# Performance work log

Hardware: AMD Instinct MI355X
Metric: run time of the kernel (lower is better)

Reference implementation:

```python
import jax, jax.numpy as jnp
import numpy as np
import math

N_HEADS = 4
GELU = lambda x: jax.nn.gelu(x, approximate=False)  # torch nn.GELU default = exact erf

def _ln(x, s, b):
    m = jnp.mean(x, axis=-1, keepdims=True)
    v = jnp.mean((x - m) ** 2, axis=-1, keepdims=True)
    return (x - m) * jax.lax.rsqrt(v + 1e-5) * s + b

def _fwd(materials, in_seq, proj_vars, param_vars, enc_w1, enc_b1, enc_w2, enc_b2, sos,
         tl_wq, tl_wk, tl_wv, tl_bq, tl_bk, tl_bv, tl_wo, tl_bo,
         tl_ln1s, tl_ln1b, tl_ln2s, tl_ln2b, tl_fw1, tl_fb1, tl_fw2, tl_fb2,
         pw1, pb1, pw2, pb2, pw3, pb3, pw4, pb4, pw5, pb5,
         ipw1, ipb1, ipw2, ipb2, hw1, hb1, hw2, hb2, hw3, hb3):
    B = in_seq.shape[0]
    # encoder input MLP: [B,S,1] -> [B,S,D]
    x = GELU(in_seq @ enc_w1 + enc_b1) @ enc_w2 + enc_b2
    x = jnp.concatenate([jnp.broadcast_to(sos, (B, 1, sos.shape[-1])), x], axis=1)
    S1, D = x.shape[1], x.shape[2]
    dh = D // N_HEADS
    # sinusoidal positional encoding
    pos = jnp.arange(S1, dtype=jnp.float32)[:, None]
    div = jnp.exp(jnp.arange(0, D, 2, dtype=jnp.float32) * (-math.log(10000.0) / D))
    ang = pos * div
    pe = jnp.stack([jnp.sin(ang), jnp.cos(ang)], axis=-1).reshape(S1, D)
    x = x + pe
    scale = 1.0 / math.sqrt(dh)
    # post-LN TransformerEncoder layers (torch default norm_first=False), eval mode (no dropout)
    for l in range(tl_wq.shape[0]):
        q = (x @ tl_wq[l] + tl_bq[l]).reshape(B, S1, N_HEADS, dh).transpose(0, 2, 1, 3)
        k = (x @ tl_wk[l] + tl_bk[l]).reshape(B, S1, N_HEADS, dh).transpose(0, 2, 1, 3)
        v = (x @ tl_wv[l] + tl_bv[l]).reshape(B, S1, N_HEADS, dh).transpose(0, 2, 1, 3)
        att = jax.nn.softmax(jnp.einsum('bhqd,bhkd->bhqk', q, k) * scale, axis=-1)
        o = jnp.einsum('bhqk,bhkd->bhqd', att, v).transpose(0, 2, 1, 3).reshape(B, S1, D)
        x = _ln(x + o @ tl_wo[l] + tl_bo[l], tl_ln1s[l], tl_ln1b[l])
        f = GELU(x @ tl_fw1[l] + tl_fb1[l]) @ tl_fw2[l] + tl_fb2[l]
        x = _ln(x + f, tl_ln2s[l], tl_ln2b[l])
    sos_out = x[:, 0]
    h = jnp.concatenate([proj_vars, sos_out], axis=1)
    for w, b in ((pw1, pb1), (pw2, pb2), (pw3, pb3), (pw4, pb4)):
        h = GELU(h @ w + b)
    proj_out = h @ pw5 + pb5
    pp = GELU(param_vars @ ipw1 + ipb1) @ ipw2 + ipb2
    mi = jnp.concatenate([pp, proj_out], axis=1)  # [B, output_features+param_vars]
    # MaterialHead mask-gather-MLP-scatter == run every tiny head densely, pick by material id
    h1 = GELU(jnp.einsum('bi,mio->mbo', mi, hw1) + hb1[:, None, :])
    h2 = GELU(jnp.einsum('mbi,mio->mbo', h1, hw2) + hb2[:, None, :])
    h3 = jnp.einsum('mbi,mio->mbo', h2, hw3) + hb3[:, None, :]  # [M,B,1]
    return h3[materials, jnp.arange(B)]  # [B,1]

def setup_inputs() -> dict:
    key = jax.random.key(0)
    ks = iter(jax.random.split(key, 64))
    def rn(shape, scale=0.05):
        return jax.random.normal(next(ks), shape, dtype=jnp.float32) * scale
    B, S, IN, EL, D, L, DFF = 64, 1024, 1, 48, 64, 3, 256
    PV, PP, OF, M = 3, 3, 24, 3
    IF = OF + PP
    return dict(
        in_seq=rn((B, S, IN), 1.0),
        proj_vars=rn((B, PV), 1.0),
        param_vars=rn((B, PP), 1.0),
        materials=jax.random.randint(next(ks), (B,), 0, M),
        enc_w1=rn((IN, EL)), enc_b1=rn((EL,)), enc_w2=rn((EL, D)), enc_b2=rn((D,)),
        sos=rn((1, 1, D)),
        tl_wq=rn((L, D, D)), tl_wk=rn((L, D, D)), tl_wv=rn((L, D, D)),
        tl_bq=rn((L, D)), tl_bk=rn((L, D)), tl_bv=rn((L, D)),
        tl_wo=rn((L, D, D)), tl_bo=rn((L, D)),
        tl_ln1s=jnp.ones((L, D)), tl_ln1b=jnp.zeros((L, D)),
        tl_ln2s=jnp.ones((L, D)), tl_ln2b=jnp.zeros((L, D)),
        tl_fw1=rn((L, D, DFF)), tl_fb1=rn((L, DFF)), tl_fw2=rn((L, DFF, D)), tl_fb2=rn((L, D)),
        pw1=rn((PV + D, 34)), pb1=rn((34,)), pw2=rn((34, 11)), pb2=rn((11,)),
        pw3=rn((11, 36)), pb3=rn((36,)), pw4=rn((36, 22)), pb4=rn((22,)),
        pw5=rn((22, OF)), pb5=rn((OF,)),
        ipw1=rn((PP, 3)), ipb1=rn((3,)), ipw2=rn((3, PP)), ipb2=rn((PP,)),
        hw1=rn((M, IF, 15)), hb1=rn((M, 15)), hw2=rn((M, 15, 18)), hb2=rn((M, 18)),
        hw3=rn((M, 18, 1)), hb3=rn((M, 1)),
    )

def reference(in_seq, proj_vars, param_vars, materials, enc_w1, enc_b1, enc_w2, enc_b2, sos,
              tl_wq, tl_wk, tl_wv, tl_bq, tl_bk, tl_bv, tl_wo, tl_bo,
              tl_ln1s, tl_ln1b, tl_ln2s, tl_ln2b, tl_fw1, tl_fb1, tl_fw2, tl_fb2,
              pw1, pb1, pw2, pb2, pw3, pb3, pw4, pb4, pw5, pb5,
              ipw1, ipb1, ipw2, ipb2, hw1, hb1, hw2, hb2, hw3, hb3):
    return _fwd(materials, in_seq, proj_vars, param_vars, enc_w1, enc_b1, enc_w2, enc_b2, sos,
                tl_wq, tl_wk, tl_wv, tl_bq, tl_bk, tl_bv, tl_wo, tl_bo,
                tl_ln1s, tl_ln1b, tl_ln2s, tl_ln2b, tl_fw1, tl_fb1, tl_fw2, tl_fb2,
                pw1, pb1, pw2, pb2, pw3, pb3, pw4, pb4, pw5, pb5,
                ipw1, ipb1, ipw2, ipb2, hw1, hb1, hw2, hb2, hw3, hb3)
```

## Files before the change

kernel.cpp:

```cpp
#include <hip/hip_runtime.h>
#include <hip/hip_bf16.h>
#include <math.h>

#define BB   64
#define SS   1024
#define S1C  1025
#define DD   64
#define NHD  4
#define NBH  (BB * NHD)
#define DHD  16
#define DFFC 256
#define NLAY 3
#define NTOK (BB * S1C)
#define SPAD 1056
#define TGRP2 9
#define FTQ   32
#define FT2   32
#define OPAD 68
#define QSCL 0.36067376022224085f

typedef const float* fp;
typedef __attribute__((ext_vector_type(8))) short bf16x8;
typedef __attribute__((ext_vector_type(4))) float f32x4;
typedef __attribute__((ext_vector_type(2))) unsigned int u32x2;
typedef __attribute__((ext_vector_type(4))) unsigned int u32x4;

#if __has_builtin(__builtin_amdgcn_exp2f)
#define RAW_EXP2(x) __builtin_amdgcn_exp2f(x)
#else
#define RAW_EXP2(x) __expf(0.6931471805599453f * (x))
#endif
#if __has_builtin(__builtin_amdgcn_rcpf)
#define RAW_RCP(x) __builtin_amdgcn_rcpf(x)
#else
#define RAW_RCP(x) (1.0f / (x))
#endif

__device__ __forceinline__ float gelu_exact(float x) {
    return 0.5f * x * (1.0f + erff(x * 0.7071067811865475f));
}
__device__ __forceinline__ float erf_fast(float x) {
    float ax = fabsf(x);
    float t = RAW_RCP(1.0f + 0.3275911f * ax);
    float p = t * (0.254829592f + t * (-0.284496736f + t * (1.421413741f +
              t * (-1.453152027f + t * 1.061405429f))));
    float e = RAW_EXP2(ax * ax * -1.4426950408889634f);
    float r = 1.0f - p * e;
    return copysignf(r, x);
}
__device__ __forceinline__ float gelu_fast(float x) {
    return 0.5f * x * (1.0f + erf_fast(x * 0.7071067811865475f));
}
__device__ __forceinline__ short f2b(float f) {
    unsigned u = __float_as_uint(f);
    return (short)((u + 0x7fffu + ((u >> 16) & 1u)) >> 16);
}

__device__ __forceinline__ u32x2 pack4exp(f32x4 c, bool valid) {
    float e0 = valid ? RAW_EXP2(c[0]) : 0.f;
    float e1 = valid ? RAW_EXP2(c[1]) : 0.f;
    float e2 = valid ? RAW_EXP2(c[2]) : 0.f;
    float e3 = valid ? RAW_EXP2(c[3]) : 0.f;
    unsigned r0, r1;
    asm("v_cvt_pk_bf16_f32 %0, %1, %2" : "=v"(r0) : "v"(e0), "v"(e1));
    asm("v_cvt_pk_bf16_f32 %0, %1, %2" : "=v"(r1) : "v"(e2), "v"(e3));
    return (u32x2){r0, r1};
}
__device__ __forceinline__ u32x2 pack4cvt(float x0, float x1, float x2, float x3) {
    unsigned r0, r1;
    asm("v_cvt_pk_bf16_f32 %0, %1, %2" : "=v"(r0) : "v"(x0), "v"(x1));
    asm("v_cvt_pk_bf16_f32 %0, %1, %2" : "=v"(r1) : "v"(x2), "v"(x3));
    return (u32x2){r0, r1};
}

__global__ __launch_bounds__(256) void k_wconv(
    fp wq, fp wk, fp wv, fp wo, fp w1, fp w2,
    short* __restrict__ wqkvT, short* __restrict__ woT,
    short* __restrict__ w1T, short* __restrict__ w2T)
{
    int l = blockIdx.y;
    int i = blockIdx.x * 256 + threadIdx.x;
    if (i < 12288) {
        int p = i >> 12, rem = i & 4095;
        int d = rem >> 6, j = rem & 63;
        fp src = (p == 0 ? wq : p == 1 ? wk : wv) + (size_t)l * 4096;
        float v = src[j * 64 + d];
        if (p == 0) v *= QSCL;
        wqkvT[(size_t)l * 12288 + i] = f2b(v);
    } else if (i < 16384) {
        int rem = i - 12288;
        woT[(size_t)l * 4096 + rem] = f2b(wo[(size_t)l * 4096 + (rem & 63) * 64 + (rem >> 6)]);
    } else if (i < 32768) {
        int rem = i - 16384;
        w1T[(size_t)l * 16384 + rem] = f2b(w1[(size_t)l * 16384 + (rem & 63) * 256 + (rem >> 6)]);
    } else {
        int rem = i - 32768;
        w2T[(size_t)l * 16384 + rem] = f2b(w2[(size_t)l * 16384 + (rem & 255) * 64 + (rem >> 8)]);
    }
}

__global__ __launch_bounds__(64) void k_zero(
    short* __restrict__ qb, short* __restrict__ kb, short* __restrict__ vbt)
{
    int bh = blockIdx.x, t = threadIdx.x;
    for (int i = t; i < 31 * 16; i += 64) {
        int r = i >> 4, c = i & 15;
        size_t idx = ((size_t)bh * SPAD + 1025 + r) * 16 + c;
        qb[idx] = 0; kb[idx] = 0;
    }
    for (int i = t; i < 16 * 31; i += 64) {
        int e = i / 31, c = i % 31;
        vbt[((size_t)bh * 16 + e) * SPAD + 1025 + c] = 0;
    }
}

__global__ __launch_bounds__(256) void k_encode(
    fp in_seq, fp enc_w1, fp enc_b1, fp enc_w2, fp enc_b2, fp sos,
    float* __restrict__ x, short* __restrict__ xb)
{
    int t = threadIdx.x;
    int w = t >> 6, d = t & 63;
    int tok = blockIdx.x * 4 + w;
    int b = tok / S1C, s = tok % S1C;
    __shared__ float e[4][48];
    float val;
    if (s == 0) {
        val = sos[d];
    } else {
        float tin = in_seq[b * SS + (s - 1)];
        if (d < 48) e[w][d] = gelu_fast(tin * enc_w1[d] + enc_b1[d]);
        float acc = enc_b2[d];
        for (int j = 0; j < 48; ++j) acc += e[w][j] * enc_w2[j * DD + d];
        val = acc;
    }
    int i2 = (d >> 1) * 2;
    float factor = RAW_EXP2((float)i2 * (-9.210340371976184f / 64.0f) * 1.4426950408889634f);
    float ang = (float)s * factor;
    val += (d & 1) ? __cosf(ang) : __sinf(ang);
    x[(size_t)tok * DD + d] = val;
    xb[(size_t)tok * DD + d] = f2b(val);
}

__global__ __launch_bounds__(256) void k_qkv(
    const short* __restrict__ xb, const short* __restrict__ wqkvT,
    fp bq, fp bk, fp bv,
    short* __restrict__ qb, short* __restrict__ kb, short* __restrict__ vbt)
{
    int blk = blockIdx.x, t = threadIdx.x;
    int tok0 = blk * FTQ;
    int w = t >> 6, l = t & 63;
    int quad = l >> 4, lo = l & 15;

    const short* xp0 = xb + ((size_t)(tok0 + lo)) * DD;
    const short* xp1 = xb + ((size_t)(tok0 + 16 + lo)) * DD;
    bf16x8 a0 = *(const bf16x8*)(xp0 + quad * 8);
    bf16x8 a1 = *(const bf16x8*)(xp0 + 32 + quad * 8);
    bf16x8 a2 = *(const bf16x8*)(xp1 + quad * 8);
    bf16x8 a3 = *(const bf16x8*)(xp1 + 32 + quad * 8);

    int n = w * 16 + lo;
    #pragma unroll
    for (int p = 0; p < 3; ++p) {
        const short* wT = wqkvT + (size_t)p * 4096 + (size_t)n * 64;
        bf16x8 b0 = *(const bf16x8*)(wT + quad * 8);
        bf16x8 b1 = *(const bf16x8*)(wT + 32 + quad * 8);
        f32x4 c0 = __builtin_amdgcn_mfma_f32_16x16x32_bf16(a0, b0, (f32x4){0,0,0,0}, 0, 0, 0);
        c0 = __builtin_amdgcn_mfma_f32_16x16x32_bf16(a1, b1, c0, 0, 0, 0);
        f32x4 c1 = __builtin_amdgcn_mfma_f32_16x16x32_bf16(a2, b0, (f32x4){0,0,0,0}, 0, 0, 0);
        c1 = __builtin_amdgcn_mfma_f32_16x16x32_bf16(a3, b1, c1, 0, 0, 0);
        float bias = (p == 0) ? bq[n] * QSCL : (p == 1) ? bk[n] : bv[n];
        #pragma unroll
        for (int r = 0; r < 4; ++r) {
            int tok = tok0 + quad * 4 + r;
            int bb0 = tok / S1C, ss0 = tok % S1C;
            int bh = bb0 * NHD + w;
            short val = f2b(c0[r] + bias);
            int tok2 = tok + 16;
            int bb1 = tok2 / S1C, ss1 = tok2 % S1C;
            int bh2 = bb1 * NHD + w;
            short val2 = f2b(c1[r] + bias);
            if (p == 0) {
                qb[((size_t)bh * SPAD + ss0) * 16 + lo] = val;
                qb[((size_t)bh2 * SPAD + ss1) * 16 + lo] = val2;
            } else if (p == 1) {
                kb[((size_t)bh * SPAD + ss0) * 16 + lo] = val;
                kb[((size_t)bh2 * SPAD + ss1) * 16 + lo] = val2;
            } else {
                vbt[((size_t)bh * 16 + lo) * SPAD + ss0] = val;
                vbt[((size_t)bh2 * 16 + lo) * SPAD + ss1] = val2;
            }
        }
    }
}

__global__ __launch_bounds__(256) void k_attn(
    const short* __restrict__ qb, const short* __restrict__ kb,
    const short* __restrict__ vbt, short* __restrict__ ob)
{
    int bid = blockIdx.x;
    int bh  = bid % NBH;
    int grp = bid / NBH;
    int b = bh >> 2, h = bh & 3;
    int t = threadIdx.x;
    int w = t >> 6, l = t & 63;
    int quad = l >> 4, lo = l & 15;
    int t0 = grp * 4 + w;
    int t1 = t0 + 36;
    if (t1 > 65) t1 = 65;
    int qg0 = t0 * 16, qg1 = t1 * 16;

    __shared__ u32x2 ptmem[4][2][272];
    char* ptc = (char*)&ptmem[w][0][0];
    unsigned ptbase = (unsigned)(uintptr_t)ptc;

    const short* qbase = qb + (size_t)bh * SPAD * 16;
    const short* kbase = kb + (size_t)bh * SPAD * 16;
    const short* vbase = vbt + (size_t)bh * 16 * SPAD;

    bf16x8 aQ0 = {0,0,0,0,0,0,0,0}, aQ1 = {0,0,0,0,0,0,0,0};
    if (quad < 2) {
        aQ0 = *(const bf16x8*)(qbase + ((size_t)(qg0 + lo)) * 16 + quad * 8);
        aQ1 = *(const bf16x8*)(qbase + ((size_t)(qg1 + lo)) * 16 + quad * 8);
    }

    const short ONE = 0x3F80;
    bf16x8 aOne = {ONE, ONE, ONE, ONE, ONE, ONE, ONE, ONE};

    f32x4 oc0 = {0.f,0.f,0.f,0.f}, oc1 = {0.f,0.f,0.f,0.f};
    f32x4 dn0 = {0.f,0.f,0.f,0.f}, dn1 = {0.f,0.f,0.f,0.f};

    unsigned wo0 = (unsigned)((lo >> 2) * 136 + (lo & 3) * 32 + quad * 8);
    unsigned ro = (unsigned)(quad * 272 + lo * 8);
    unsigned rd0 = ptbase + ro;
    unsigned rd1 = ptbase + 2176 + ro;
    char* wb0 = ptc + wo0;
    char* wb1 = ptc + 2176 + wo0;

    bf16x8 kxA, kyA, kxB, kyB, vA, vB;

    {
        const short* k0p = kbase + (size_t)lo * 16 + (quad & 1) * 8;
        kxA = *(const bf16x8*)k0p;
        kyA = *(const bf16x8*)(k0p + 256);
        vA  = *(const bf16x8*)(vbase + (size_t)lo * SPAD + quad * 8);
        const short* k1p = kbase + (size_t)(32 + lo) * 16 + (quad & 1) * 8;
        kxB = *(const bf16x8*)k1p;
        kyB = *(const bf16x8*)(k1p + 256);

        f32x4 c0 = __builtin_amdgcn_mfma_f32_16x16x32_bf16(aQ0, kxA, (f32x4){0.f,0.f,0.f,0.f}, 0, 0, 0);
        f32x4 c1 = __builtin_amdgcn_mfma_f32_16x16x32_bf16(aQ1, kxA, (f32x4){0.f,0.f,0.f,0.f}, 0, 0, 0);
        *(u32x2*)(wb0)        = pack4exp(c0, true);
        *(u32x2*)(wb0 + 1088) = pack4exp(c1, true);
        c0 = __builtin_amdgcn_mfma_f32_16x16x32_bf16(aQ0, kyA, (f32x4){0.f,0.f,0.f,0.f}, 0, 0, 0);
        c1 = __builtin_amdgcn_mfma_f32_16x16x32_bf16(aQ1, kyA, (f32x4){0.f,0.f,0.f,0.f}, 0, 0, 0);
        *(u32x2*)(wb0 + 544)  = pack4exp(c0, true);
        *(u32x2*)(wb0 + 1632) = pack4exp(c1, true);
    }

#define STEP(CH, TAIL, KXC, KYC, KXN, KYN, VP, VC, RD, WB) do {               \
    int ch_ = (CH);                                                            \
    if (!(TAIL)) {                                                             \
        const short* kn_ = kbase + (size_t)((ch_ + 1) * 32 + lo) * 16 + (quad & 1) * 8; \
        KXN = *(const bf16x8*)kn_;                                             \
        KYN = *(const bf16x8*)(kn_ + 256);                                     \
    }                                                                          \
    VC = *(const bf16x8*)(vbase + (size_t)lo * SPAD + ch_ * 32 + quad * 8);    \
    u32x2 p00_, p01_, p10_, p11_;                                              \
    asm volatile("ds_read_b64_tr_b16 %0, %1"             : "=v"(p00_) : "v"(RD) : "memory"); \
    asm volatile("ds_read_b64_tr_b16 %0, %1 offset:136"  : "=v"(p01_) : "v"(RD) : "memory"); \
    asm volatile("ds_read_b64_tr_b16 %0, %1 offset:1088" : "=v"(p10_) : "v"(RD) : "memory"); \
    asm volatile("ds_read_b64_tr_b16 %0, %1 offset:1224" : "=v"(p11_) : "v"(RD) : "memory"); \
    u32x2 wA0_, wA1_, wB0_, wB1_;                                              \
    {                                                                          \
        f32x4 c0_ = __builtin_amdgcn_mfma_f32_16x16x32_bf16(aQ0, KXC, (f32x4){0.f,0.f,0.f,0.f}, 0, 0, 0); \
        f32x4 c1_ = __builtin_amdgcn_mfma_f32_16x16x32_bf16(aQ1, KXC, (f32x4){0.f,0.f,0.f,0.f}, 0, 0, 0); \
        bool v0_ = !(TAIL) || (lo == 0);                                       \
        wA0_ = pack4exp(c0_, v0_);                                             \
        wB0_ = pack4exp(c1_, v0_);                                             \
        c0_ = __builtin_amdgcn_mfma_f32_16x16x32_bf16(aQ0, KYC, (f32x4){0.f,0.f,0.f,0.f}, 0, 0, 0); \
        c1_ = __builtin_amdgcn_mfma_f32_16x16x32_bf16(aQ1, KYC, (f32x4){0.f,0.f,0.f,0.f}, 0, 0, 0); \
        bool v1_ = !(TAIL);                                                    \
        wA1_ = pack4exp(c0_, v1_);                                             \
        wB1_ = pack4exp(c1_, v1_);                                             \
    }                                                                          \
    asm volatile("s_waitcnt lgkmcnt(0)" ::: "memory");                         \
    __builtin_amdgcn_sched_barrier(0);                                         \
    u32x4 q0_; q0_[0] = p00_[0]; q0_[1] = p00_[1]; q0_[2] = p01_[0]; q0_[3] = p01_[1]; \
    u32x4 q1_; q1_[0] = p10_[0]; q1_[1] = p10_[1]; q1_[2] = p11_[0]; q1_[3] = p11_[1]; \
    bf16x8 pB0_ = __builtin_bit_cast(bf16x8, q0_);                             \
    bf16x8 pB1_ = __builtin_bit_cast(bf16x8, q1_);                             \
    oc0 = __builtin_amdgcn_mfma_f32_16x16x32_bf16(VP, pB0_, oc0, 0, 0, 0);     \
    dn0 = __builtin_amdgcn_mfma_f32_16x16x32_bf16(aOne, pB0_, dn0, 0, 0, 0);   \
    oc1 = __builtin_amdgcn_mfma_f32_16x16x32_bf16(VP, pB1_, oc1, 0, 0, 0);     \
    dn1 = __builtin_amdgcn_mfma_f32_16x16x32_bf16(aOne, pB1_, dn1, 0, 0, 0);   \
    *(u32x2*)((WB))        = wA0_;                                             \
    *(u32x2*)((WB) + 1088) = wB0_;                                             \
    *(u32x2*)((WB) + 544)  = wA1_;                                             \
    *(u32x2*)((WB) + 1632) = wB1_;                                             \
} while (0)

    for (int chp = 1; chp < 31; chp += 2) {
        STEP(chp,     0, kxA, kyA, kxB, kyB, vA, vB, rd0, wb1);
        STEP(chp + 1, 0, kxB, kyB, kxA, kyA, vB, vA, rd1, wb0);
    }
    STEP(31, 0, kxA, kyA, kxB, kyB, vA, vB, rd0, wb1);
    STEP(32, 1, kxB, kyB, kxA, kyA, vB, vA, rd1, wb0);
#undef STEP

    {
        u32x2 p00, p01, p10, p11;
        asm volatile("ds_read_b64_tr_b16 %0, %1"             : "=v"(p00) : "v"(rd0) : "memory");
        asm volatile("ds_read_b64_tr_b16 %0, %1 offset:136"  : "=v"(p01) : "v"(rd0) : "memory");
        asm volatile("ds_read_b64_tr_b16 %0, %1 offset:1088" : "=v"(p10) : "v"(rd0) : "memory");
        asm volatile("ds_read_b64_tr_b16 %0, %1 offset:1224" : "=v"(p11) : "v"(rd0) : "memory");
        asm volatile("s_waitcnt lgkmcnt(0)" ::: "memory");
        __builtin_amdgcn_sched_barrier(0);
        u32x4 q0; q0[0] = p00[0]; q0[1] = p00[1]; q0[2] = p01[0]; q0[3] = p01[1];
        u32x4 q1; q1[0] = p10[0]; q1[1] = p10[1]; q1[2] = p11[0]; q1[3] = p11[1];
        bf16x8 pB0 = __builtin_bit_cast(bf16x8, q0);
        bf16x8 pB1 = __builtin_bit_cast(bf16x8, q1);
        oc0 = __builtin_amdgcn_mfma_f32_16x16x32_bf16(vA, pB0, oc0, 0, 0, 0);
        dn0 = __builtin_amdgcn_mfma_f32_16x16x32_bf16(aOne, pB0, dn0, 0, 0, 0);
        oc1 = __builtin_amdgcn_mfma_f32_16x16x32_bf16(vA, pB1, oc1, 0, 0, 0);
        dn1 = __builtin_amdgcn_mfma_f32_16x16x32_bf16(aOne, pB1, dn1, 0, 0, 0);
    }

    {
        int qrow = qg0 + lo;
        if (qrow < S1C) {
            float inv = 1.0f / dn0[0];
            unsigned p0 = (unsigned short)f2b(oc0[0] * inv) | ((unsigned)(unsigned short)f2b(oc0[1] * inv) << 16);
            unsigned p1 = (unsigned short)f2b(oc0[2] * inv) | ((unsigned)(unsigned short)f2b(oc0[3] * inv) << 16);
            *(uint2*)(ob + ((size_t)b * S1C + qrow) * DD + h * DHD + quad * 4) = make_uint2(p0, p1);
        }
    }
    {
        int qrow = qg1 + lo;
        if (qrow < S1C) {
            float inv = 1.0f / dn1[0];
            unsigned p0 = (unsigned short)f2b(oc1[0] * inv) | ((unsigned)(unsigned short)f2b(oc1[1] * inv) << 16);
            unsigned p1 = (unsigned short)f2b(oc1[2] * inv) | ((unsigned)(unsigned short)f2b(oc1[3] * inv) << 16);
            *(uint2*)(ob + ((size_t)b * S1C + qrow) * DD + h * DHD + quad * 4) = make_uint2(p0, p1);
        }
    }
}

__global__ __launch_bounds__(256) void k_block(
    const short* __restrict__ ob, float* __restrict__ x,
    const short* __restrict__ woT, fp bo, fp ln1s, fp ln1b,
    const short* __restrict__ w1T, fp b1, const short* __restrict__ w2T, fp b2,
    fp ln2s, fp ln2b,
    const short* __restrict__ wqkvTn, fp bqn, fp bkn, fp bvn,
    short* __restrict__ qb, short* __restrict__ kb, short* __restrict__ vbt,
    int has_next)
{
    int blk = blockIdx.x, t = threadIdx.x;
    int tok0 = blk * FT2;
    int w = t >> 6, l = t & 63;
    int quad = l >> 4, lo = l & 15;

    __shared__ float otf[FT2][OPAD];
    __shared__ u32x2 hidtr[2][8][136];
    short* ysb = (short*)&otf[0][0];
    char*  hidc = (char*)&hidtr[0][0][0];
    unsigned hidbase = (unsigned)(uintptr_t)hidc;

    int tt8 = t >> 3;
    int d8s = (t & 7) * 8;
    const float* xrow = x + (size_t)(tok0 + tt8) * DD + d8s;
    float4 xpa = *(const float4*)xrow;
    float4 xpb = *(const float4*)(xrow + 4);
    float4 s1a = *(const float4*)(ln1s + d8s);
    float4 s1b = *(const float4*)(ln1s + d8s + 4);
    float4 b1a = *(const float4*)(ln1b + d8s);
    float4 b1b = *(const float4*)(ln1b + d8s + 4);

    {
        const short* obp0 = ob + ((size_t)(tok0 + lo)) * DD;
        const short* obp1 = ob + ((size_t)(tok0 + 16 + lo)) * DD;
        bf16x8 a0 = *(const bf16x8*)(obp0 + quad * 8);
        bf16x8 a1 = *(const bf16x8*)(obp0 + 32 + quad * 8);
        bf16x8 a2 = *(const bf16x8*)(obp1 + quad * 8);
        bf16x8 a3 = *(const bf16x8*)(obp1 + 32 + quad * 8);
        int n = w * 16 + lo;
        const short* wT = woT + (size_t)n * 64;
        bf16x8 b0 = *(const bf16x8*)(wT + quad * 8);
        bf16x8 bb = *(const bf16x8*)(wT + 32 + quad * 8);
        f32x4 c0 = __builtin_amdgcn_mfma_f32_16x16x32_bf16(a0, b0, (f32x4){0,0,0,0}, 0, 0, 0);
        c0 = __builtin_amdgcn_mfma_f32_16x16x32_bf16(a1, bb, c0, 0, 0, 0);
        f32x4 c1 = __builtin_amdgcn_mfma_f32_16x16x32_bf16(a2, b0, (f32x4){0,0,0,0}, 0, 0, 0);
        c1 = __builtin_amdgcn_mfma_f32_16x16x32_bf16(a3, bb, c1, 0, 0, 0);
        float bov = bo[n];
        #pragma unroll
        for (int r = 0; r < 4; ++r) {
            otf[quad * 4 + r][n] = c0[r] + bov;
            otf[16 + quad * 4 + r][n] = c1[r] + bov;
        }
    }
    __syncthreads();

    float yv[8];
    {
        float4 o0 = *(const float4*)&otf[tt8][d8s];
        float4 o1 = *(const float4*)&otf[tt8][d8s + 4];
        float v0 = o0.x + xpa.x, v1 = o0.y + xpa.y, v2 = o0.z + xpa.z, v3 = o0.w + xpa.w;
        float v4 = o1.x + xpb.x, v5 = o1.y + xpb.y, v6 = o1.z + xpb.z, v7 = o1.w + xpb.w;
        float sum = ((v0 + v1) + (v2 + v3)) + ((v4 + v5) + (v6 + v7));
        float vs = v0 * v0;
        vs = fmaf(v1, v1, vs); vs = fmaf(v2, v2, vs); vs = fmaf(v3, v3, vs);
        vs = fmaf(v4, v4, vs); vs = fmaf(v5, v5, vs); vs = fmaf(v6, v6, vs);
        vs = fmaf(v7, v7, vs);
        sum += __shfl_xor(sum, 1, 64); sum += __shfl_xor(sum, 2, 64); sum += __shfl_xor(sum, 4, 64);
        vs  += __shfl_xor(vs , 1, 64); vs  += __shfl_xor(vs , 2, 64); vs  += __shfl_xor(vs , 4, 64);
        float mean = sum * (1.0f / 64.0f);
        float var = vs * (1.0f / 64.0f) - mean * mean;
        float rs = rsqrtf(var + 1e-5f);
        yv[0] = (v0 - mean) * rs * s1a.x + b1a.x;
        yv[1] = (v1 - mean) * rs * s1a.y + b1a.y;
        yv[2] = (v2 - mean) * rs * s1a.z + b1a.z;
        yv[3] = (v3 - mean) * rs * s1a.w + b1a.w;
        yv[4] = (v4 - mean) * rs * s1b.x + b1b.x;
        yv[5] = (v5 - mean) * rs * s1b.y + b1b.y;
        yv[6] = (v6 - mean) * rs * s1b.z + b1b.z;
        yv[7] = (v7 - mean) * rs * s1b.w + b1b.w;
        u32x2 pa = pack4cvt(yv[0], yv[1], yv[2], yv[3]);
        u32x2 pb = pack4cvt(yv[4], yv[5], yv[6], yv[7]);
        *(u32x4*)&ysb[tt8 * 136 + d8s] = (u32x4){pa[0], pa[1], pb[0], pb[1]};
    }
    __syncthreads();

    {
        bf16x8 a0 = *(const bf16x8*)&ysb[(size_t)lo * 136 + quad * 8];
        bf16x8 a1 = *(const bf16x8*)&ysb[(size_t)lo * 136 + 32 + quad * 8];
        bf16x8 a2 = *(const bf16x8*)&ysb[(size_t)(16 + lo) * 136 + quad * 8];
        bf16x8 a3 = *(const bf16x8*)&ysb[(size_t)(16 + lo) * 136 + 32 + quad * 8];
        unsigned hoff = (unsigned)(w * 2176 + (lo >> 2) * 136 + (lo & 3) * 32 + quad * 8);
        #pragma unroll
        for (int i = 0; i < 4; ++i) {
            int n = w * 64 + i * 16 + lo;
            const short* wT = w1T + (size_t)n * 64;
            bf16x8 b0 = *(const bf16x8*)(wT + quad * 8);
            bf16x8 bb = *(const bf16x8*)(wT + 32 + quad * 8);
            f32x4 c0 = __builtin_amdgcn_mfma_f32_16x16x32_bf16(a0, b0, (f32x4){0,0,0,0}, 0, 0, 0);
            c0 = __builtin_amdgcn_mfma_f32_16x16x32_bf16(a1, bb, c0, 0, 0, 0);
            f32x4 c1 = __builtin_amdgcn_mfma_f32_16x16x32_bf16(a2, b0, (f32x4){0,0,0,0}, 0, 0, 0);
            c1 = __builtin_amdgcn_mfma_f32_16x16x32_bf16(a3, bb, c1, 0, 0, 0);
            float b1v = b1[n];
            unsigned off = hoff + (i >> 1) * 1088 + (i & 1) * 544;
            *(u32x2*)(hidc + off) = pack4cvt(
                gelu_fast(c0[0] + b1v), gelu_fast(c0[1] + b1v),
                gelu_fast(c0[2] + b1v), gelu_fast(c0[3] + b1v));
            *(u32x2*)(hidc + 8704 + off) = pack4cvt(
                gelu_fast(c1[0] + b1v), gelu_fast(c1[1] + b1v),
                gelu_fast(c1[2] + b1v), gelu_fast(c1[3] + b1v));
        }
    }
    __syncthreads();

    {
        f32x4 c20 = {0.f,0.f,0.f,0.f}, c21 = {0.f,0.f,0.f,0.f};
        const short* wT2 = w2T + (size_t)(w * 16 + lo) * 256;
        unsigned ro = (unsigned)(quad * 272 + lo * 8);
        unsigned tb0 = hidbase + ro;
        unsigned tb1 = hidbase + 8704 + ro;
        u32x2 pA0, pA1, pA2, pA3, pB0, pB1, pB2, pB3;

#define TRRD(dst, addr, OFFSTR) \
    asm volatile("ds_read_b64_tr_b16 %0, %1 offset:" OFFSTR : "=v"(dst) : "v"(addr))
#define ISS(P0,P1,P2,P3, O1, O2) \
    TRRD(P0, tb0, O1); TRRD(P1, tb0, O2); TRRD(P2, tb1, O1); TRRD(P3, tb1, O2)
#define W4 asm volatile("s_waitcnt lgkmcnt(4)" ::: "memory"); __builtin_amdgcn_sched_barrier(0)
#define W0 asm volatile("s_waitcnt lgkmcnt(0)" ::: "memory"); __builtin_amdgcn_sched_barrier(0)
#define CONS(P0,P1,P2,P3, BF) do { \
    u32x4 q0_; q0_[0]=P0[0]; q0_[1]=P0[1]; q0_[2]=P1[0]; q0_[3]=P1[1]; \
    u32x4 q1_; q1_[0]=P2[0]; q1_[1]=P2[1]; q1_[2]=P3[0]; q1_[3]=P3[1]; \
    c20 = __builtin_amdgcn_mfma_f32_16x16x32_bf16(__builtin_bit_cast(bf16x8,q0_), BF, c20, 0,0,0); \
    c21 = __builtin_amdgcn_mfma_f32_16x16x32_bf16(__builtin_bit_cast(bf16x8,q1_), BF, c21, 0,0,0); \
} while (0)

        bf16x8 bfA = *(const bf16x8*)(wT2 + quad * 8);
        ISS(pA0,pA1,pA2,pA3, "0",    "136");
        bf16x8 bfB = *(const bf16x8*)(wT2 + 32 + quad * 8);
        ISS(pB0,pB1,pB2,pB3, "1088", "1224");
        W4; CONS(pA0,pA1,pA2,pA3, bfA);
        bfA = *(const bf16x8*)(wT2 + 64 + quad * 8);
        ISS(pA0,pA1,pA2,pA3, "2176", "2312");
        W4; CONS(pB0,pB1,pB2,pB3, bfB);
        bfB = *(const bf16x8*)(wT2 + 96 + quad * 8);
        ISS(pB0,pB1,pB2,pB3, "3264", "3400");
        W4; CONS(pA0,pA1,pA2,pA3, bfA);
        bfA = *(const bf16x8*)(wT2 + 128 + quad * 8);
        ISS(pA0,pA1,pA2,pA3, "4352", "4488");
        W4; CONS(pB0,pB1,pB2,pB3, bfB);
        bfB = *(const bf16x8*)(wT2 + 160 + quad * 8);
        ISS(pB0,pB1,pB2,pB3, "5440", "5576");
        W4; CONS(pA0,pA1,pA2,pA3, bfA);
        bfA = *(const bf16x8*)(wT2 + 192 + quad * 8);
        ISS(pA0,pA1,pA2,pA3, "6528", "6664");
        W4; CONS(pB0,pB1,pB2,pB3, bfB);
        bfB = *(const bf16x8*)(wT2 + 224 + quad * 8);
        ISS(pB0,pB1,pB2,pB3, "7616", "7752");
        W4; CONS(pA0,pA1,pA2,pA3, bfA);
        W0; CONS(pB0,pB1,pB2,pB3, bfB);
#undef TRRD
#undef ISS
#undef W4
#undef W0
#undef CONS

        float b2v = b2[w * 16 + lo];
        #pragma unroll
        for (int r = 0; r < 4; ++r) {
            otf[quad * 4 + r][w * 16 + lo] = c20[r] + b2v;
            otf[16 + quad * 4 + r][w * 16 + lo] = c21[r] + b2v;
        }
    }
    __syncthreads();

    {
        float4 s2a = *(const float4*)(ln2s + d8s);
        float4 s2b = *(const float4*)(ln2s + d8s + 4);
        float4 b2a = *(const float4*)(ln2b + d8s);
        float4 b2b = *(const float4*)(ln2b + d8s + 4);
        float4 o0 = *(const float4*)&otf[tt8][d8s];
        float4 o1 = *(const float4*)&otf[tt8][d8s + 4];
        float v0 = o0.x + yv[0], v1 = o0.y + yv[1], v2 = o0.z + yv[2], v3 = o0.w + yv[3];
        float v4 = o1.x + yv[4], v5 = o1.y + yv[5], v6 = o1.z + yv[6], v7 = o1.w + yv[7];
        float sum = ((v0 + v1) + (v2 + v3)) + ((v4 + v5) + (v6 + v7));
        float vs = v0 * v0;
        vs = fmaf(v1, v1, vs); vs = fmaf(v2, v2, vs); vs = fmaf(v3, v3, vs);
        vs = fmaf(v4, v4, vs); vs = fmaf(v5, v5, vs); vs = fmaf(v6, v6, vs);
        vs = fmaf(v7, v7, vs);
        sum += __shfl_xor(sum, 1, 64); sum += __shfl_xor(sum, 2, 64); sum += __shfl_xor(sum, 4, 64);
        vs  += __shfl_xor(vs , 1, 64); vs  += __shfl_xor(vs , 2, 64); vs  += __shfl_xor(vs , 4, 64);
        float mean = sum * (1.0f / 64.0f);
        float var = vs * (1.0f / 64.0f) - mean * mean;
        float rs = rsqrtf(var + 1e-5f);
        float y0 = (v0 - mean) * rs * s2a.x + b2a.x;
        float y1 = (v1 - mean) * rs * s2a.y + b2a.y;
        float y2 = (v2 - mean) * rs * s2a.z + b2a.z;
        float y3 = (v3 - mean) * rs * s2a.w + b2a.w;
        float y4 = (v4 - mean) * rs * s2b.x + b2b.x;
        float y5 = (v5 - mean) * rs * s2b.y + b2b.y;
        float y6 = (v6 - mean) * rs * s2b.z + b2b.z;
        float y7 = (v7 - mean) * rs * s2b.w + b2b.w;
        float* xo = x + (size_t)(tok0 + tt8) * DD + d8s;
        *(float4*)xo = make_float4(y0, y1, y2, y3);
        *(float4*)(xo + 4) = make_float4(y4, y5, y6, y7);
        u32x2 pa = pack4cvt(y0, y1, y2, y3);
        u32x2 pb = pack4cvt(y4, y5, y6, y7);
        *(u32x4*)&ysb[tt8 * 136 + d8s] = (u32x4){pa[0], pa[1], pb[0], pb[1]};
    }
    __syncthreads();

    if (has_next) {
        bf16x8 a0 = *(const bf16x8*)&ysb[(size_t)lo * 136 + quad * 8];
        bf16x8 a1 = *(const bf16x8*)&ysb[(size_t)lo * 136 + 32 + quad * 8];
        bf16x8 a2 = *(const bf16x8*)&ysb[(size_t)(16 + lo) * 136 + quad * 8];
        bf16x8 a3 = *(const bf16x8*)&ysb[(size_t)(16 + lo) * 136 + 32 + quad * 8];
        int n = w * 16 + lo;
        #pragma unroll
        for (int p = 0; p < 3; ++p) {
            const short* wT = wqkvTn + (size_t)p * 4096 + (size_t)n * 64;
            bf16x8 b0 = *(const bf16x8*)(wT + quad * 8);
            bf16x8 bb = *(const bf16x8*)(wT + 32 + quad * 8);
            f32x4 c0 = __builtin_amdgcn_mfma_f32_16x16x32_bf16(a0, b0, (f32x4){0,0,0,0}, 0, 0, 0);
            c0 = __builtin_amdgcn_mfma_f32_16x16x32_bf16(a1, bb, c0, 0, 0, 0);
            f32x4 c1 = __builtin_amdgcn_mfma_f32_16x16x32_bf16(a2, b0, (f32x4){0,0,0,0}, 0, 0, 0);
            c1 = __builtin_amdgcn_mfma_f32_16x16x32_bf16(a3, bb, c1, 0, 0, 0);
            float bias = (p == 0) ? bqn[n] * QSCL : (p == 1) ? bkn[n] : bvn[n];
            #pragma unroll
            for (int r = 0; r < 4; ++r) {
                int tok = tok0 + quad * 4 + r;
                int bb0 = tok / S1C, ss0 = tok % S1C;
                int bh = bb0 * NHD + w;
                short val = f2b(c0[r] + bias);
                int tok2 = tok + 16;
                int bb1 = tok2 / S1C, ss1 = tok2 % S1C;
                int bh2 = bb1 * NHD + w;
                short val2 = f2b(c1[r] + bias);
                if (p == 0) {
                    qb[((size_t)bh * SPAD + ss0) * 16 + lo] = val;
                    qb[((size_t)bh2 * SPAD + ss1) * 16 + lo] = val2;
                } else if (p == 1) {
                    kb[((size_t)bh * SPAD + ss0) * 16 + lo] = val;
                    kb[((size_t)bh2 * SPAD + ss1) * 16 + lo] = val2;
                } else {
                    vbt[((size_t)bh * 16 + lo) * SPAD + ss0] = val;
                    vbt[((size_t)bh2 * 16 + lo) * SPAD + ss1] = val2;
                }
            }
        }
    }
}

__global__ __launch_bounds__(64) void k_head(
    const float* __restrict__ x, fp proj_vars, fp param_vars,
    const int* __restrict__ materials,
    fp pw1, fp pb1, fp pw2, fp pb2, fp pw3, fp pb3,
    fp pw4, fp pb4, fp pw5, fp pb5,
    fp ipw1, fp ipb1, fp ipw2, fp ipb2,
    fp hw1, fp hb1, fp hw2, fp hb2, fp hw3, fp hb3,
    float* __restrict__ out)
{
    int b = blockIdx.x;
    int tid = threadIdx.x;
    __shared__ float A[80], Bf[80], pp[8], mi[32];

    if (tid < 3) A[tid] = proj_vars[b * 3 + tid];
    A[3 + tid] = x[((size_t)b * S1C + 0) * DD + tid];
    __syncthreads();

    if (tid < 34) {
        float a = pb1[tid];
        for (int i = 0; i < 67; ++i) a += A[i] * pw1[i * 34 + tid];
        Bf[tid] = gelu_exact(a);
    }
    __syncthreads();
    if (tid < 11) {
        float a = pb2[tid];
        for (int i = 0; i < 34; ++i) a += Bf[i] * pw2[i * 11 + tid];
        A[tid] = gelu_exact(a);
    }
    __syncthreads();
    if (tid < 36) {
        float a = pb3[tid];
        for (int i = 0; i < 11; ++i) a += A[i] * pw3[i * 36 + tid];
        Bf[tid] = gelu_exact(a);
    }
    __syncthreads();
    if (tid < 22) {
        float a = pb4[tid];
        for (int i = 0; i < 36; ++i) a += Bf[i] * pw4[i * 22 + tid];
        A[tid] = gelu_exact(a);
    }
    __syncthreads();
    if (tid < 24) {
        float a = pb5[tid];
        for (int i = 0; i < 22; ++i) a += A[i] * pw5[i * 24 + tid];
        mi[3 + tid] = a;
    }
    if (tid < 3) {
        float a = ipb1[tid];
        for (int i = 0; i < 3; ++i) a += param_vars[b * 3 + i] * ipw1[i * 3 + tid];
        pp[tid] = gelu_exact(a);
    }
    __syncthreads();
    if (tid < 3) {
        float a = ipb2[tid];
        for (int i = 0; i < 3; ++i) a += pp[i] * ipw2[i * 3 + tid];
        mi[tid] = a;
    }
    __syncthreads();

    int m = materials[b];
    if (tid < 15) {
        float a = hb1[m * 15 + tid];
        for (int i = 0; i < 27; ++i) a += mi[i] * hw1[(m * 27 + i) * 15 + tid];
        A[tid] = gelu_exact(a);
    }
    __syncthreads();
    if (tid < 18) {
        float a = hb2[m * 18 + tid];
        for (int i = 0; i < 15; ++i) a += A[i] * hw2[(m * 15 + i) * 18 + tid];
        Bf[tid] = gelu_exact(a);
    }
    __syncthreads();
    if (tid == 0) {
        float a = hb3[m];
        for (int i = 0; i < 18; ++i) a += Bf[i] * hw3[m * 18 + i];
        out[b] = a;
    }
}

extern "C" void kernel_launch(void* const* d_in, const int* in_sizes, int n_in,
                              void* d_out, int out_size, void* d_ws, size_t ws_size,
                              hipStream_t stream) {
    fp in_seq     = (fp)d_in[0];
    fp proj_vars  = (fp)d_in[1];
    fp param_vars = (fp)d_in[2];
    const int* materials = (const int*)d_in[3];
    fp enc_w1 = (fp)d_in[4];
    fp enc_b1 = (fp)d_in[5];
    fp enc_w2 = (fp)d_in[6];
    fp enc_b2 = (fp)d_in[7];
    fp sos    = (fp)d_in[8];
    fp tl_wq  = (fp)d_in[9];
    fp tl_wk  = (fp)d_in[10];
    fp tl_wv  = (fp)d_in[11];
    fp tl_bq  = (fp)d_in[12];
    fp tl_bk  = (fp)d_in[13];
    fp tl_bv  = (fp)d_in[14];
    fp tl_wo  = (fp)d_in[15];
    fp tl_bo  = (fp)d_in[16];
    fp tl_ln1s = (fp)d_in[17];
    fp tl_ln1b = (fp)d_in[18];
    fp tl_ln2s = (fp)d_in[19];
    fp tl_ln2b = (fp)d_in[20];
    fp tl_fw1 = (fp)d_in[21];
    fp tl_fb1 = (fp)d_in[22];
    fp tl_fw2 = (fp)d_in[23];
    fp tl_fb2 = (fp)d_in[24];
    fp pw1 = (fp)d_in[25]; fp pb1 = (fp)d_in[26];
    fp pw2 = (fp)d_in[27]; fp pb2 = (fp)d_in[28];
    fp pw3 = (fp)d_in[29]; fp pb3 = (fp)d_in[30];
    fp pw4 = (fp)d_in[31]; fp pb4 = (fp)d_in[32];
    fp pw5 = (fp)d_in[33]; fp pb5 = (fp)d_in[34];
    fp ipw1 = (fp)d_in[35]; fp ipb1 = (fp)d_in[36];
    fp ipw2 = (fp)d_in[37]; fp ipb2 = (fp)d_in[38];
    fp hw1 = (fp)d_in[39]; fp hb1 = (fp)d_in[40];
    fp hw2 = (fp)d_in[41]; fp hb2 = (fp)d_in[42];
    fp hw3 = (fp)d_in[43]; fp hb3 = (fp)d_in[44];

    float* x  = (float*)d_ws;
    short* ob = (short*)(x + (size_t)NTOK * DD);
    short* xb = ob + (size_t)NTOK * DD;
    short* qb = xb + (size_t)NTOK * DD;
    short* kb = qb + (size_t)NBH * SPAD * 16;
    short* vbt = kb + (size_t)NBH * SPAD * 16;
    short* wqkvT = vbt + (size_t)NBH * 16 * SPAD;
    short* woT = wqkvT + (size_t)NLAY * 12288;
    short* w1T = woT + (size_t)NLAY * 4096;
    short* w2T = w1T + (size_t)NLAY * 16384;

    k_wconv<<<dim3(192, NLAY), 256, 0, stream>>>(
        tl_wq, tl_wk, tl_wv, tl_wo, tl_fw1, tl_fw2, wqkvT, woT, w1T, w2T);
    k_zero<<<NBH, 64, 0, stream>>>(qb, kb, vbt);
    k_encode<<<NTOK / 4, 256, 0, stream>>>(in_seq, enc_w1, enc_b1, enc_w2, enc_b2, sos, x, xb);

    k_qkv<<<NTOK / FTQ, 256, 0, stream>>>(
        xb, wqkvT,
        tl_bq, tl_bk, tl_bv,
        qb, kb, vbt);

    for (int l = 0; l < NLAY; ++l) {
        k_attn<<<NBH * TGRP2, 256, 0, stream>>>(qb, kb, vbt, ob);
        int ln = (l + 1 < NLAY) ? (l + 1) : l;
        k_block<<<NTOK / FT2, 256, 0, stream>>>(
            ob, x,
            woT + (size_t)l * 4096, tl_bo + (size_t)l * DD,
            tl_ln1s + (size_t)l * DD, tl_ln1b + (size_t)l * DD,
            w1T + (size_t)l * 16384, tl_fb1 + (size_t)l * DFFC,
            w2T + (size_t)l * 16384, tl_fb2 + (size_t)l * DD,
            tl_ln2s + (size_t)l * DD, tl_ln2b + (size_t)l * DD,
            wqkvT + (size_t)ln * 12288,
            tl_bq + (size_t)ln * DD, tl_bk + (size_t)ln * DD, tl_bv + (size_t)ln * DD,
            qb, kb, vbt,
            (l + 1 < NLAY) ? 1 : 0);
    }

    k_head<<<BB, 64, 0, stream>>>(
        x, proj_vars, param_vars, materials,
        pw1, pb1, pw2, pb2, pw3, pb3, pw4, pb4, pw5, pb5,
        ipw1, ipb1, ipw2, ipb2,
        hw1, hb1, hw2, hb2, hw3, hb3,
        (float*)d_out);
}
```

Measured before the change: 477.8 us.

## Give each attention wave three query tiles and fuse encoder with QKV projection

```diff
diff --git a/kernel.cpp b/kernel.cpp
--- a/kernel.cpp
+++ b/kernel.cpp
@@ -13,7 +13,7 @@
 #define NLAY 3
 #define NTOK (BB * S1C)
 #define SPAD 1056
-#define TGRP2 9
+#define TGRP3 6
 #define FTQ   32
 #define FT2   32
 #define OPAD 68
@@ -114,49 +114,47 @@
     }
 }
 
-__global__ __launch_bounds__(256) void k_encode(
+__global__ __launch_bounds__(256) void k_encqkv(
     fp in_seq, fp enc_w1, fp enc_b1, fp enc_w2, fp enc_b2, fp sos,
-    float* __restrict__ x, short* __restrict__ xb)
+    const short* __restrict__ wqkvT, fp bq, fp bk, fp bv,
+    float* __restrict__ x,
+    short* __restrict__ qb, short* __restrict__ kb, short* __restrict__ vbt)
 {
     int t = threadIdx.x;
+    int tok0 = blockIdx.x * FTQ;
     int w = t >> 6, d = t & 63;
-    int tok = blockIdx.x * 4 + w;
-    int b = tok / S1C, s = tok % S1C;
     __shared__ float e[4][48];
-    float val;
-    if (s == 0) {
-        val = sos[d];
-    } else {
-        float tin = in_seq[b * SS + (s - 1)];
-        if (d < 48) e[w][d] = gelu_fast(tin * enc_w1[d] + enc_b1[d]);
-        float acc = enc_b2[d];
-        for (int j = 0; j < 48; ++j) acc += e[w][j] * enc_w2[j * DD + d];
-        val = acc;
-    }
+    __shared__ short xs[FTQ][72];
+
     int i2 = (d >> 1) * 2;
     float factor = RAW_EXP2((float)i2 * (-9.210340371976184f / 64.0f) * 1.4426950408889634f);
-    float ang = (float)s * factor;
-    val += (d & 1) ? __cosf(ang) : __sinf(ang);
-    x[(size_t)tok * DD + d] = val;
-    xb[(size_t)tok * DD + d] = f2b(val);
-}
-
-__global__ __launch_bounds__(256) void k_qkv(
-    const short* __restrict__ xb, const short* __restrict__ wqkvT,
-    fp bq, fp bk, fp bv,
-    short* __restrict__ qb, short* __restrict__ kb, short* __restrict__ vbt)
-{
-    int blk = blockIdx.x, t = threadIdx.x;
-    int tok0 = blk * FTQ;
-    int w = t >> 6, l = t & 63;
+    for (int i = 0; i < 8; ++i) {
+        int tl = i * 4 + w;
+        int tok = tok0 + tl;
+        int b = tok / S1C, s = tok % S1C;
+        float val;
+        if (s == 0) {
+            val = sos[d];
+        } else {
+            float tin = in_seq[b * SS + (s - 1)];
+            if (d < 48) e[w][d] = gelu_fast(tin * enc_w1[d] + enc_b1[d]);
+            float acc = enc_b2[d];
+            for (int j = 0; j < 48; ++j) acc += e[w][j] * enc_w2[j * DD + d];
+            val = acc;
+        }
+        float ang = (float)s * factor;
+        val += (d & 1) ? __cosf(ang) : __sinf(ang);
+        x[(size_t)tok * DD + d] = val;
+        xs[tl][d] = f2b(val);
+    }
+    __syncthreads();
+
+    int l = t & 63;
     int quad = l >> 4, lo = l & 15;
-
-    const short* xp0 = xb + ((size_t)(tok0 + lo)) * DD;
-    const short* xp1 = xb + ((size_t)(tok0 + 16 + lo)) * DD;
-    bf16x8 a0 = *(const bf16x8*)(xp0 + quad * 8);
-    bf16x8 a1 = *(const bf16x8*)(xp0 + 32 + quad * 8);
-    bf16x8 a2 = *(const bf16x8*)(xp1 + quad * 8);
-    bf16x8 a3 = *(const bf16x8*)(xp1 + 32 + quad * 8);
+    bf16x8 a0 = *(const bf16x8*)&xs[lo][quad * 8];
+    bf16x8 a1 = *(const bf16x8*)&xs[lo][32 + quad * 8];
+    bf16x8 a2 = *(const bf16x8*)&xs[16 + lo][quad * 8];
+    bf16x8 a3 = *(const bf16x8*)&xs[16 + lo][32 + quad * 8];
 
     int n = w * 16 + lo;
     #pragma unroll
@@ -205,11 +203,12 @@
     int w = t >> 6, l = t & 63;
     int quad = l >> 4, lo = l & 15;
     int t0 = grp * 4 + w;
-    int t1 = t0 + 36;
-    if (t1 > 65) t1 = 65;
-    int qg0 = t0 * 16, qg1 = t1 * 16;
-
-    __shared__ u32x2 ptmem[4][2][272];
+    if (t0 > 21) t0 = 21;
+    int t1 = t0 + 22;
+    int t2 = t0 + 44;
+    int qg0 = t0 * 16, qg1 = t1 * 16, qg2 = t2 * 16;
+
+    __shared__ u32x2 ptmem[4][2][408];
     char* ptc = (char*)&ptmem[w][0][0];
     unsigned ptbase = (unsigned)(uintptr_t)ptc;
 
@@ -217,24 +216,25 @@
     const short* kbase = kb + (size_t)bh * SPAD * 16;
     const short* vbase = vbt + (size_t)bh * 16 * SPAD;
 
-    bf16x8 aQ0 = {0,0,0,0,0,0,0,0}, aQ1 = {0,0,0,0,0,0,0,0};
+    bf16x8 aQ0 = {0,0,0,0,0,0,0,0}, aQ1 = {0,0,0,0,0,0,0,0}, aQ2 = {0,0,0,0,0,0,0,0};
     if (quad < 2) {
         aQ0 = *(const bf16x8*)(qbase + ((size_t)(qg0 + lo)) * 16 + quad * 8);
         aQ1 = *(const bf16x8*)(qbase + ((size_t)(qg1 + lo)) * 16 + quad * 8);
+        aQ2 = *(const bf16x8*)(qbase + ((size_t)(qg2 + lo)) * 16 + quad * 8);
     }
 
     const short ONE = 0x3F80;
     bf16x8 aOne = {ONE, ONE, ONE, ONE, ONE, ONE, ONE, ONE};
 
-    f32x4 oc0 = {0.f,0.f,0.f,0.f}, oc1 = {0.f,0.f,0.f,0.f};
-    f32x4 dn0 = {0.f,0.f,0.f,0.f}, dn1 = {0.f,0.f,0.f,0.f};
+    f32x4 oc0 = {0.f,0.f,0.f,0.f}, oc1 = {0.f,0.f,0.f,0.f}, oc2 = {0.f,0.f,0.f,0.f};
+    f32x4 dn0 = {0.f,0.f,0.f,0.f}, dn1 = {0.f,0.f,0.f,0.f}, dn2 = {0.f,0.f,0.f,0.f};
 
     unsigned wo0 = (unsigned)((lo >> 2) * 136 + (lo & 3) * 32 + quad * 8);
     unsigned ro = (unsigned)(quad * 272 + lo * 8);
     unsigned rd0 = ptbase + ro;
-    unsigned rd1 = ptbase + 2176 + ro;
+    unsigned rd1 = ptbase + 3264 + ro;
     char* wb0 = ptc + wo0;
-    char* wb1 = ptc + 2176 + wo0;
+    char* wb1 = ptc + 3264 + wo0;
 
     bf16x8 kxA, kyA, kxB, kyB, vA, vB;
 
@@ -249,12 +249,16 @@
 
         f32x4 c0 = __builtin_amdgcn_mfma_f32_16x16x32_bf16(aQ0, kxA, (f32x4){0.f,0.f,0.f,0.f}, 0, 0, 0);
         f32x4 c1 = __builtin_amdgcn_mfma_f32_16x16x32_bf16(aQ1, kxA, (f32x4){0.f,0.f,0.f,0.f}, 0, 0, 0);
+        f32x4 c2 = __builtin_amdgcn_mfma_f32_16x16x32_bf16(aQ2, kxA, (f32x4){0.f,0.f,0.f,0.f}, 0, 0, 0);
         *(u32x2*)(wb0)        = pack4exp(c0, true);
         *(u32x2*)(wb0 + 1088) = pack4exp(c1, true);
+        *(u32x2*)(wb0 + 2176) = pack4exp(c2, true);
         c0 = __builtin_amdgcn_mfma_f32_16x16x32_bf16(aQ0, kyA, (f32x4){0.f,0.f,0.f,0.f}, 0, 0, 0);
         c1 = __builtin_amdgcn_mfma_f32_16x16x32_bf16(aQ1, kyA, (f32x4){0.f,0.f,0.f,0.f}, 0, 0, 0);
+        c2 = __builtin_amdgcn_mfma_f32_16x16x32_bf16(aQ2, kyA, (f32x4){0.f,0.f,0.f,0.f}, 0, 0, 0);
         *(u32x2*)(wb0 + 544)  = pack4exp(c0, true);
         *(u32x2*)(wb0 + 1632) = pack4exp(c1, true);
+        *(u32x2*)(wb0 + 2720) = pack4exp(c2, true);
     }
 
 #define STEP(CH, TAIL, KXC, KYC, KXN, KYN, VP, VC, RD, WB) do {               \
@@ -265,38 +269,50 @@
         KYN = *(const bf16x8*)(kn_ + 256);                                     \
     }                                                                          \
     VC = *(const bf16x8*)(vbase + (size_t)lo * SPAD + ch_ * 32 + quad * 8);    \
-    u32x2 p00_, p01_, p10_, p11_;                                              \
+    u32x2 p00_, p01_, p10_, p11_, p20_, p21_;                                  \
     asm volatile("ds_read_b64_tr_b16 %0, %1"             : "=v"(p00_) : "v"(RD) : "memory"); \
     asm volatile("ds_read_b64_tr_b16 %0, %1 offset:136"  : "=v"(p01_) : "v"(RD) : "memory"); \
     asm volatile("ds_read_b64_tr_b16 %0, %1 offset:1088" : "=v"(p10_) : "v"(RD) : "memory"); \
     asm volatile("ds_read_b64_tr_b16 %0, %1 offset:1224" : "=v"(p11_) : "v"(RD) : "memory"); \
-    u32x2 wA0_, wA1_, wB0_, wB1_;                                              \
+    asm volatile("ds_read_b64_tr_b16 %0, %1 offset:2176" : "=v"(p20_) : "v"(RD) : "memory"); \
+    asm volatile("ds_read_b64_tr_b16 %0, %1 offset:2312" : "=v"(p21_) : "v"(RD) : "memory"); \
+    u32x2 wt0x_, wt1x_, wt2x_, wt0y_, wt1y_, wt2y_;                            \
     {                                                                          \
         f32x4 c0_ = __builtin_amdgcn_mfma_f32_16x16x32_bf16(aQ0, KXC, (f32x4){0.f,0.f,0.f,0.f}, 0, 0, 0); \
         f32x4 c1_ = __builtin_amdgcn_mfma_f32_16x16x32_bf16(aQ1, KXC, (f32x4){0.f,0.f,0.f,0.f}, 0, 0, 0); \
+        f32x4 c2_ = __builtin_amdgcn_mfma_f32_16x16x32_bf16(aQ2, KXC, (f32x4){0.f,0.f,0.f,0.f}, 0, 0, 0); \
         bool v0_ = !(TAIL) || (lo == 0);                                       \
-        wA0_ = pack4exp(c0_, v0_);                                             \
-        wB0_ = pack4exp(c1_, v0_);                                             \
+        wt0x_ = pack4exp(c0_, v0_);                                            \
+        wt1x_ = pack4exp(c1_, v0_);                                            \
+        wt2x_ = pack4exp(c2_, v0_);                                            \
         c0_ = __builtin_amdgcn_mfma_f32_16x16x32_bf16(aQ0, KYC, (f32x4){0.f,0.f,0.f,0.f}, 0, 0, 0); \
         c1_ = __builtin_amdgcn_mfma_f32_16x16x32_bf16(aQ1, KYC, (f32x4){0.f,0.f,0.f,0.f}, 0, 0, 0); \
+        c2_ = __builtin_amdgcn_mfma_f32_16x16x32_bf16(aQ2, KYC, (f32x4){0.f,0.f,0.f,0.f}, 0, 0, 0); \
         bool v1_ = !(TAIL);                                                    \
-        wA1_ = pack4exp(c0_, v1_);                                             \
-        wB1_ = pack4exp(c1_, v1_);                                             \
+        wt0y_ = pack4exp(c0_, v1_);                                            \
+        wt1y_ = pack4exp(c1_, v1_);                                            \
+        wt2y_ = pack4exp(c2_, v1_);                                            \
     }                                                                          \
     asm volatile("s_waitcnt lgkmcnt(0)" ::: "memory");                         \
     __builtin_amdgcn_sched_barrier(0);                                         \
     u32x4 q0_; q0_[0] = p00_[0]; q0_[1] = p00_[1]; q0_[2] = p01_[0]; q0_[3] = p01_[1]; \
     u32x4 q1_; q1_[0] = p10_[0]; q1_[1] = p10_[1]; q1_[2] = p11_[0]; q1_[3] = p11_[1]; \
+    u32x4 q2_; q2_[0] = p20_[0]; q2_[1] = p20_[1]; q2_[2] = p21_[0]; q2_[3] = p21_[1]; \
     bf16x8 pB0_ = __builtin_bit_cast(bf16x8, q0_);                             \
     bf16x8 pB1_ = __builtin_bit_cast(bf16x8, q1_);                             \
+    bf16x8 pB2_ = __builtin_bit_cast(bf16x8, q2_);                             \
     oc0 = __builtin_amdgcn_mfma_f32_16x16x32_bf16(VP, pB0_, oc0, 0, 0, 0);     \
     dn0 = __builtin_amdgcn_mfma_f32_16x16x32_bf16(aOne, pB0_, dn0, 0, 0, 0);   \
     oc1 = __builtin_amdgcn_mfma_f32_16x16x32_bf16(VP, pB1_, oc1, 0, 0, 0);     \
     dn1 = __builtin_amdgcn_mfma_f32_16x16x32_bf16(aOne, pB1_, dn1, 0, 0, 0);   \
-    *(u32x2*)((WB))        = wA0_;                                             \
-    *(u32x2*)((WB) + 1088) = wB0_;                                             \
-    *(u32x2*)((WB) + 544)  = wA1_;                                             \
-    *(u32x2*)((WB) + 1632) = wB1_;                                             \
+    oc2 = __builtin_amdgcn_mfma_f32_16x16x32_bf16(VP, pB2_, oc2, 0, 0, 0);     \
+    dn2 = __builtin_amdgcn_mfma_f32_16x16x32_bf16(aOne, pB2_, dn2, 0, 0, 0);   \
+    *(u32x2*)((WB))        = wt0x_;                                            \
+    *(u32x2*)((WB) + 544)  = wt0y_;                                            \
+    *(u32x2*)((WB) + 1088) = wt1x_;                                            \
+    *(u32x2*)((WB) + 1632) = wt1y_;                                            \
+    *(u32x2*)((WB) + 2176) = wt2x_;                                            \
+    *(u32x2*)((WB) + 2720) = wt2y_;                                            \
 } while (0)
 
     for (int chp = 1; chp < 31; chp += 2) {
@@ -308,21 +324,27 @@
 #undef STEP
 
     {
-        u32x2 p00, p01, p10, p11;
+        u32x2 p00, p01, p10, p11, p20, p21;
         asm volatile("ds_read_b64_tr_b16 %0, %1"             : "=v"(p00) : "v"(rd0) : "memory");
         asm volatile("ds_read_b64_tr_b16 %0, %1 offset:136"  : "=v"(p01) : "v"(rd0) : "memory");
         asm volatile("ds_read_b64_tr_b16 %0, %1 offset:1088" : "=v"(p10) : "v"(rd0) : "memory");
         asm volatile("ds_read_b64_tr_b16 %0, %1 offset:1224" : "=v"(p11) : "v"(rd0) : "memory");
+        asm volatile("ds_read_b64_tr_b16 %0, %1 offset:2176" : "=v"(p20) : "v"(rd0) : "memory");
+        asm volatile("ds_read_b64_tr_b16 %0, %1 offset:2312" : "=v"(p21) : "v"(rd0) : "memory");
         asm volatile("s_waitcnt lgkmcnt(0)" ::: "memory");
         __builtin_amdgcn_sched_barrier(0);
         u32x4 q0; q0[0] = p00[0]; q0[1] = p00[1]; q0[2] = p01[0]; q0[3] = p01[1];
         u32x4 q1; q1[0] = p10[0]; q1[1] = p10[1]; q1[2] = p11[0]; q1[3] = p11[1];
+        u32x4 q2; q2[0] = p20[0]; q2[1] = p20[1]; q2[2] = p21[0]; q2[3] = p21[1];
         bf16x8 pB0 = __builtin_bit_cast(bf16x8, q0);
         bf16x8 pB1 = __builtin_bit_cast(bf16x8, q1);
+        bf16x8 pB2 = __builtin_bit_cast(bf16x8, q2);
         oc0 = __builtin_amdgcn_mfma_f32_16x16x32_bf16(vA, pB0, oc0, 0, 0, 0);
         dn0 = __builtin_amdgcn_mfma_f32_16x16x32_bf16(aOne, pB0, dn0, 0, 0, 0);
         oc1 = __builtin_amdgcn_mfma_f32_16x16x32_bf16(vA, pB1, oc1, 0, 0, 0);
         dn1 = __builtin_amdgcn_mfma_f32_16x16x32_bf16(aOne, pB1, dn1, 0, 0, 0);
+        oc2 = __builtin_amdgcn_mfma_f32_16x16x32_bf16(vA, pB2, oc2, 0, 0, 0);
+        dn2 = __builtin_amdgcn_mfma_f32_16x16x32_bf16(aOne, pB2, dn2, 0, 0, 0);
     }
 
     {
@@ -340,6 +362,15 @@
             float inv = 1.0f / dn1[0];
             unsigned p0 = (unsigned short)f2b(oc1[0] * inv) | ((unsigned)(unsigned short)f2b(oc1[1] * inv) << 16);
             unsigned p1 = (unsigned short)f2b(oc1[2] * inv) | ((unsigned)(unsigned short)f2b(oc1[3] * inv) << 16);
+            *(uint2*)(ob + ((size_t)b * S1C + qrow) * DD + h * DHD + quad * 4) = make_uint2(p0, p1);
+        }
+    }
+    {
+        int qrow = qg2 + lo;
+        if (qrow < S1C) {
+            float inv = 1.0f / dn2[0];
+            unsigned p0 = (unsigned short)f2b(oc2[0] * inv) | ((unsigned)(unsigned short)f2b(oc2[1] * inv) << 16);
+            unsigned p1 = (unsigned short)f2b(oc2[2] * inv) | ((unsigned)(unsigned short)f2b(oc2[3] * inv) << 16);
             *(uint2*)(ob + ((size_t)b * S1C + qrow) * DD + h * DHD + quad * 4) = make_uint2(p0, p1);
         }
     }
@@ -726,15 +757,13 @@
     k_wconv<<<dim3(192, NLAY), 256, 0, stream>>>(
         tl_wq, tl_wk, tl_wv, tl_wo, tl_fw1, tl_fw2, wqkvT, woT, w1T, w2T);
     k_zero<<<NBH, 64, 0, stream>>>(qb, kb, vbt);
-    k_encode<<<NTOK / 4, 256, 0, stream>>>(in_seq, enc_w1, enc_b1, enc_w2, enc_b2, sos, x, xb);
-
-    k_qkv<<<NTOK / FTQ, 256, 0, stream>>>(
-        xb, wqkvT,
-        tl_bq, tl_bk, tl_bv,
-        qb, kb, vbt);
+    k_encqkv<<<NTOK / FTQ, 256, 0, stream>>>(
+        in_seq, enc_w1, enc_b1, enc_w2, enc_b2, sos,
+        wqkvT, tl_bq, tl_bk, tl_bv,
+        x, qb, kb, vbt);
 
     for (int l = 0; l < NLAY; ++l) {
-        k_attn<<<NBH * TGRP2, 256, 0, stream>>>(qb, kb, vbt, ob);
+        k_attn<<<NBH * TGRP3, 256, 0, stream>>>(qb, kb, vbt, ob);
         int ln = (l + 1 < NLAY) ? (l + 1) : l;
         k_block<<<NTOK / FT2, 256, 0, stream>>>(
             ob, x,
```

After: 474.0 us. Within noise of the previous version (-0.8%).
